# Optimization experiments

Hardware: AMD Instinct MI355X
Metric: run time of the kernel (lower is better)

The kernel has to match this reference:

```python
import jax, jax.numpy as jnp
import numpy as np

N_HEAD = 16

def setup_inputs() -> dict:
    key = jax.random.key(0)
    ks = jax.random.split(key, 5)
    d = 1024
    x = jax.random.normal(ks[0], (2, 2048, d), dtype=jnp.float32)
    Wqkv = jax.random.normal(ks[1], (d, 3 * d), dtype=jnp.float32) * (1.0 / np.sqrt(d))
    bqkv = jnp.zeros((3 * d,), dtype=jnp.float32)
    Wproj = jax.random.normal(ks[2], (d, d), dtype=jnp.float32) * (1.0 / np.sqrt(d))
    bproj = jnp.zeros((d,), dtype=jnp.float32)
    return {"x": x, "Wqkv": Wqkv, "bqkv": bqkv, "Wproj": Wproj, "bproj": bproj}


def reference(x, Wqkv, bqkv, Wproj, bproj):
    B, T, C = x.shape
    H = N_HEAD
    Dh = C // H
    qkv = x @ Wqkv + bqkv                      # [B, T, 3C]
    q, k, v = jnp.split(qkv, 3, axis=-1)
    # [B, T, C] -> [B, H, T, Dh]
    q = q.reshape(B, T, H, Dh).transpose(0, 2, 1, 3)
    k = k.reshape(B, T, H, Dh).transpose(0, 2, 1, 3)
    v = v.reshape(B, T, H, Dh).transpose(0, 2, 1, 3)
    scale = 1.0 / np.sqrt(Dh)
    att = jnp.einsum('bhqd,bhkd->bhqk', q, k) * scale
    causal = jnp.tril(jnp.ones((T, T), dtype=bool))
    att = jnp.where(causal[None, None, :, :], att, jnp.float32(-jnp.inf))
    att = jax.nn.softmax(att, axis=-1)
    y = jnp.einsum('bhqk,bhkd->bhqd', att, v)  # [B, H, T, Dh]
    y = y.transpose(0, 2, 1, 3).reshape(B, T, C)
    return y @ Wproj + bproj
```

## Files before the change

### kernel.cpp

```cpp
#include <hip/hip_runtime.h>
#include <math.h>


typedef __attribute__((ext_vector_type(8))) short short8;
typedef __attribute__((ext_vector_type(4))) short short4v;
typedef __attribute__((ext_vector_type(4))) float floatx4;

__device__ __forceinline__ unsigned short f2bf(float f) {
  unsigned u = __float_as_uint(f);
  return (unsigned short)((u + 0x7fff + ((u >> 16) & 1)) >> 16);
}

__device__ __forceinline__ void pack_a_body(const float* __restrict__ in,
                                            unsigned short* __restrict__ out,
                                            int K, int m0, int k0,
                                            unsigned short (*lds)[72], int t) {
  {
    int ml = t >> 2, kl = (t & 3) * 16;
    const float4* p = (const float4*)(in + (size_t)(m0 + ml) * K + k0 + kl);
    unsigned short* q = &lds[ml][kl];
#pragma unroll
    for (int c = 0; c < 4; ++c) {
      float4 v = p[c];
      q[c * 4 + 0] = f2bf(v.x);
      q[c * 4 + 1] = f2bf(v.y);
      q[c * 4 + 2] = f2bf(v.z);
      q[c * 4 + 3] = f2bf(v.w);
    }
  }
  __syncthreads();
  int chunk = t >> 3, sub = t & 7;
  int mt = chunk >> 3, kc = chunk & 7;
  unsigned short tmp[16];
#pragma unroll
  for (int j2 = 0; j2 < 2; ++j2)
#pragma unroll
    for (int j = 0; j < 8; ++j)
      tmp[j2 * 8 + j] = lds[mt * 16 + sub * 2 + j2][kc * 8 + j];
  size_t ofs = ((size_t)(m0 >> 4) + mt) * (16 * (size_t)K) +
               ((size_t)(k0 >> 3) + kc) * 128 + sub * 16;
  *(int4*)(out + ofs) = *(int4*)(tmp);
  *(int4*)(out + ofs + 8) = *(int4*)(tmp + 8);
}

__device__ __forceinline__ void pack_bt_body(const float* __restrict__ in,
                                             unsigned short* __restrict__ out,
                                             int K, int N, int n0, int k0,
                                             unsigned short (*lds)[72], int t) {
  {
    int kl = t >> 2, nl = (t & 3) * 16;
    const float4* p = (const float4*)(in + (size_t)(k0 + kl) * N + n0 + nl);
#pragma unroll
    for (int c = 0; c < 4; ++c) {
      float4 v = p[c];
      lds[nl + c * 4 + 0][kl] = f2bf(v.x);
      lds[nl + c * 4 + 1][kl] = f2bf(v.y);
      lds[nl + c * 4 + 2][kl] = f2bf(v.z);
      lds[nl + c * 4 + 3][kl] = f2bf(v.w);
    }
  }
  __syncthreads();
  int chunk = t >> 3, sub = t & 7;
  int nt = chunk >> 3, kc = chunk & 7;
  unsigned short tmp[16];
#pragma unroll
  for (int j2 = 0; j2 < 2; ++j2)
#pragma unroll
    for (int j = 0; j < 8; ++j)
      tmp[j2 * 8 + j] = lds[nt * 16 + sub * 2 + j2][kc * 8 + j];
  size_t ofs = ((size_t)(n0 >> 4) + nt) * (16 * (size_t)K) +
               ((size_t)(k0 >> 3) + kc) * 128 + sub * 16;
  *(int4*)(out + ofs) = *(int4*)(tmp);
  *(int4*)(out + ofs + 8) = *(int4*)(tmp + 8);
}

__global__ __launch_bounds__(256) void pack_all(
    const float* __restrict__ x, const float* __restrict__ Wqkv,
    const float* __restrict__ Wproj, unsigned short* __restrict__ xbf,
    unsigned short* __restrict__ wqkvF, unsigned short* __restrict__ wprojF) {
  __shared__ __align__(16) unsigned short lds[64][72];
  const int b = blockIdx.x, t = threadIdx.x;
  if (b < 1024) {
    pack_a_body(x, xbf, 1024, (b >> 4) * 64, (b & 15) * 64, lds, t);
  } else if (b < 1792) {
    int b2 = b - 1024;
    pack_bt_body(Wqkv, wqkvF, 1024, 3072, (b2 % 48) * 64, (b2 / 48) * 64, lds, t);
  } else {
    int b3 = b - 1792;
    pack_bt_body(Wproj, wprojF, 1024, 1024, (b3 & 15) * 64, (b3 >> 4) * 64, lds, t);
  }
}

template <int MODE, int IM>
__global__ __launch_bounds__(256) void gemm_frag(
    const unsigned short* __restrict__ A, const unsigned short* __restrict__ B,
    const float* __restrict__ bias, float* __restrict__ Cout,
    unsigned short* __restrict__ Qb, unsigned short* __restrict__ Kb,
    unsigned short* __restrict__ Vt, int M, int N, int K) {
  const int tid = threadIdx.x;
  const int wave = tid >> 6, lane = tid & 63;
  const int quad = lane >> 4, l15 = lane & 15;
  const int nbands = M / (IM * 16);
  const int band = (int)(blockIdx.x % nbands);
  const int grp = (int)(blockIdx.x / nbands);
  const int m0 = band * (IM * 16);
  const int n0 = (grp * 4 + wave) * 64;
  const int lofs = quad * 128 + l15 * 8;

  const unsigned short* pA[IM];
  const unsigned short* pB[4];
#pragma unroll
  for (int im = 0; im < IM; ++im)
    pA[im] = A + ((size_t)(m0 >> 4) + im) * (16 * (size_t)K) + lofs;
#pragma unroll
  for (int in = 0; in < 4; ++in)
    pB[in] = B + ((size_t)(n0 >> 4) + in) * (16 * (size_t)K) + lofs;

  floatx4 acc[IM][4];
#pragma unroll
  for (int i = 0; i < IM; ++i)
#pragma unroll
    for (int j = 0; j < 4; ++j) acc[i][j] = (floatx4)0.0f;

  const int nk = K >> 6;
  short8 fa[IM][2], fb[4][2], ga[IM][2], gb[4][2];

#pragma unroll
  for (int im = 0; im < IM; ++im) {
    fa[im][0] = *(const short8*)(pA[im]);
    fa[im][1] = *(const short8*)(pA[im] + 512);
  }
#pragma unroll
  for (int in = 0; in < 4; ++in) {
    fb[in][0] = *(const short8*)(pB[in]);
    fb[in][1] = *(const short8*)(pB[in] + 512);
  }

  for (int ki = 0; ki < nk; ki += 2) {
#pragma unroll
    for (int im = 0; im < IM; ++im) {
      ga[im][0] = *(const short8*)(pA[im] + 1024);
      ga[im][1] = *(const short8*)(pA[im] + 1536);
    }
#pragma unroll
    for (int in = 0; in < 4; ++in) {
      gb[in][0] = *(const short8*)(pB[in] + 1024);
      gb[in][1] = *(const short8*)(pB[in] + 1536);
    }
#pragma unroll
    for (int ks = 0; ks < 2; ++ks)
#pragma unroll
      for (int im = 0; im < IM; ++im)
#pragma unroll
        for (int in = 0; in < 4; ++in)
          acc[im][in] = __builtin_amdgcn_mfma_f32_16x16x32_bf16(
              fa[im][ks], fb[in][ks], acc[im][in], 0, 0, 0);
#pragma unroll
    for (int im = 0; im < IM; ++im) pA[im] += 2048;
#pragma unroll
    for (int in = 0; in < 4; ++in) pB[in] += 2048;
    if (ki + 2 < nk) {
#pragma unroll
      for (int im = 0; im < IM; ++im) {
        fa[im][0] = *(const short8*)(pA[im]);
        fa[im][1] = *(const short8*)(pA[im] + 512);
      }
#pragma unroll
      for (int in = 0; in < 4; ++in) {
        fb[in][0] = *(const short8*)(pB[in]);
        fb[in][1] = *(const short8*)(pB[in] + 512);
      }
    }
#pragma unroll
    for (int ks = 0; ks < 2; ++ks)
#pragma unroll
      for (int im = 0; im < IM; ++im)
#pragma unroll
        for (int in = 0; in < 4; ++in)
          acc[im][in] = __builtin_amdgcn_mfma_f32_16x16x32_bf16(
              ga[im][ks], gb[in][ks], acc[im][in], 0, 0, 0);
  }

  if (MODE == 0) {
    const float QSCALE = 0.18033688f;
#pragma unroll
    for (int im = 0; im < IM; ++im) {
      int mbase = m0 + im * 16 + quad * 4;
      int bb = mbase >> 11, tb = mbase & 2047;
#pragma unroll
      for (int in = 0; in < 4; ++in) {
        int n = n0 + in * 16 + l15;
        float bv = bias[n];
        int which = n >> 10;
        int h = (n >> 6) & 15;
        int d = n & 63;
        size_t bh_ = (size_t)(bb * 16 + h);
        if (which == 2) {
          size_t base = bh_ * 131072 + (size_t)(d >> 4) * 32768 +
                        (size_t)(tb >> 3) * 128 + (d & 15) * 8 + (tb & 7);
          short4v pk;
#pragma unroll
          for (int r = 0; r < 4; ++r) pk[r] = (short)f2bf(acc[im][in][r] + bv);
          *(short4v*)(Vt + base) = pk;
        } else {
          size_t base = bh_ * 131072 + (size_t)(tb >> 4) * 1024 +
                        (d >> 3) * 128 + (tb & 15) * 8 + (d & 7);
          if (which == 0) {
#pragma unroll
            for (int r = 0; r < 4; ++r)
              Qb[base + r * 8] = f2bf((acc[im][in][r] + bv) * QSCALE);
          } else {
#pragma unroll
            for (int r = 0; r < 4; ++r)
              Kb[base + r * 8] = f2bf(acc[im][in][r] + bv);
          }
        }
      }
    }
  } else {
#pragma unroll
    for (int im = 0; im < IM; ++im) {
      int mbase = m0 + im * 16 + quad * 4;
#pragma unroll
      for (int in = 0; in < 4; ++in) {
        int n = n0 + in * 16 + l15;
        float bv = bias[n];
#pragma unroll
        for (int r = 0; r < 4; ++r)
          Cout[(size_t)(mbase + r) * N + n] = acc[im][in][r] + bv;
      }
    }
  }
}

__global__ __launch_bounds__(256) void attn_mfma(
    const unsigned short* __restrict__ Q, const unsigned short* __restrict__ K,
    const unsigned short* __restrict__ Vt, unsigned short* __restrict__ Y) {
  const int bh = blockIdx.x;
  const int wave = threadIdx.x >> 6;
  const int lane = threadIdx.x & 63;
  const int s = ((int)(gridDim.y - 1 - blockIdx.y)) * 4 + wave;
  const int quad = lane >> 4, l15 = lane & 15;

  __shared__ __align__(16) unsigned short Plds[4][16][72];
  unsigned short(*P)[72] = Plds[wave];

  const int t0 = s * 16;
  const unsigned short* Qb = Q + (size_t)bh * 131072;
  const unsigned short* Kb = K + (size_t)bh * 131072;
  const unsigned short* Vb = Vt + (size_t)bh * 131072;
  const int lofs = quad * 128 + l15 * 8;

  short8 qf[2];
#pragma unroll
  for (int c = 0; c < 2; ++c)
    qf[c] = *(const short8*)(Qb + (size_t)s * 1024 + c * 512 + lofs);

  floatx4 o[4];
#pragma unroll
  for (int in = 0; in < 4; ++in) o[in] = (floatx4)0.0f;
  float l_acc = 0.f;

  const int ntiles = (s >> 2) + 1;

  short8 kf[4][2], vf[4][2];
#pragma unroll
  for (int in = 0; in < 4; ++in) {
    const unsigned short* kp = Kb + (size_t)in * 1024 + lofs;
    kf[in][0] = *(const short8*)(kp);
    kf[in][1] = *(const short8*)(kp + 512);
  }

  for (int jt = 0; jt < ntiles; ++jt) {
    const int kt0 = jt * 64;
#pragma unroll
    for (int in = 0; in < 4; ++in) {
      const unsigned short* vp =
          Vb + (size_t)in * 32768 + (size_t)jt * 1024 + lofs;
      vf[in][0] = *(const short8*)(vp);
      vf[in][1] = *(const short8*)(vp + 512);
    }

    floatx4 sa[4];
#pragma unroll
    for (int in = 0; in < 4; ++in) {
      floatx4 z = (floatx4)0.0f;
      z = __builtin_amdgcn_mfma_f32_16x16x32_bf16(kf[in][0], qf[0], z, 0, 0, 0);
      sa[in] = __builtin_amdgcn_mfma_f32_16x16x32_bf16(kf[in][1], qf[1], z, 0, 0, 0);
    }

    if (jt + 1 < ntiles) {
#pragma unroll
      for (int in = 0; in < 4; ++in) {
        const unsigned short* kp = Kb + (size_t)(jt * 4 + 4 + in) * 1024 + lofs;
        kf[in][0] = *(const short8*)(kp);
        kf[in][1] = *(const short8*)(kp + 512);
      }
    }

    if (jt == ntiles - 1) {
#pragma unroll
      for (int in = 0; in < 4; ++in) {
        int keyb = kt0 + in * 16 + quad * 4;
#pragma unroll
        for (int r = 0; r < 4; ++r)
          if (keyb + r > t0 + l15) sa[in][r] = -__builtin_inff();
      }
    }

#pragma unroll
    for (int in = 0; in < 4; ++in)
#pragma unroll
      for (int r = 0; r < 4; ++r) {
        float p = exp2f(sa[in][r]);
        sa[in][r] = p;
        l_acc += p;
      }

#pragma unroll
    for (int in = 0; in < 4; ++in) {
      uint2 pk;
      pk.x = (__float_as_uint(sa[in][0]) >> 16) |
             (__float_as_uint(sa[in][1]) & 0xFFFF0000u);
      pk.y = (__float_as_uint(sa[in][2]) >> 16) |
             (__float_as_uint(sa[in][3]) & 0xFFFF0000u);
      *(uint2*)&P[l15][in * 16 + quad * 4] = pk;
    }
    short8 pf0 = *(const short8*)&P[l15][quad * 8];
    short8 pf1 = *(const short8*)&P[l15][32 + quad * 8];

#pragma unroll
    for (int in = 0; in < 4; ++in) {
      o[in] = __builtin_amdgcn_mfma_f32_16x16x32_bf16(pf0, vf[in][0], o[in], 0, 0, 0);
      o[in] = __builtin_amdgcn_mfma_f32_16x16x32_bf16(pf1, vf[in][1], o[in], 0, 0, 0);
    }
  }

  l_acc += __shfl_xor(l_acc, 16);
  l_acc += __shfl_xor(l_acc, 32);

  const int b_ = bh >> 4, h = bh & 15;
  float inv[4];
#pragma unroll
  for (int r = 0; r < 4; ++r)
    inv[r] = 1.f / __shfl(l_acc, (lane & 48) | (quad * 4 + r));

  size_t mt = (size_t)(b_ * 128 + s);
#pragma unroll
  for (int in = 0; in < 4; ++in) {
    size_t cbase = (size_t)(h * 8 + in * 2 + (l15 >> 3)) * 128 + (l15 & 7);
#pragma unroll
    for (int r = 0; r < 4; ++r)
      Y[mt * 16384 + cbase + (quad * 4 + r) * 8] = f2bf(o[in][r] * inv[r]);
  }
}

extern "C" void kernel_launch(void* const* d_in, const int* in_sizes, int n_in,
                              void* d_out, int out_size, void* d_ws,
                              size_t ws_size, hipStream_t stream) {
  const float* x = (const float*)d_in[0];
  const float* Wqkv = (const float*)d_in[1];
  const float* bqkv = (const float*)d_in[2];
  const float* Wproj = (const float*)d_in[3];
  const float* bproj = (const float*)d_in[4];
  float* out = (float*)d_out;

  const int C = 1024;
  const int M = 4096;

  char* ws = (char*)d_ws;
  unsigned short* qbuf = (unsigned short*)ws;
  unsigned short* kbuf = (unsigned short*)(ws + 8388608);
  unsigned short* vtbuf = (unsigned short*)(ws + 16777216);
  unsigned short* ybuf = (unsigned short*)(ws + 25165824);
  unsigned short* xbf = (unsigned short*)(ws + 33554432);
  unsigned short* wqkvF = (unsigned short*)(ws + 41943040);
  unsigned short* wprojF = (unsigned short*)(ws + 48234496);

  dim3 blk(256);
  pack_all<<<dim3(2048), blk, 0, stream>>>(x, Wqkv, Wproj, xbf, wqkvF, wprojF);
  gemm_frag<0, 4><<<dim3((M / 64) * (3 * C / 256)), blk, 0, stream>>>(
      xbf, wqkvF, bqkv, nullptr, qbuf, kbuf, vtbuf, M, 3 * C, C);
  attn_mfma<<<dim3(32, 32), blk, 0, stream>>>(qbuf, kbuf, vtbuf, ybuf);
  gemm_frag<1, 2><<<dim3((M / 32) * (C / 256)), blk, 0, stream>>>(
      ybuf, wprojF, bproj, out, nullptr, nullptr, nullptr, M, C, C);
}
```

Before: 189.3 us.

## Stage GEMM tiles through LDS with direct global-to-LDS loads and XCD-aware mapping

Replaces the register-only fragment GEMM, where each wave loaded its own A and B fragments from global memory, with a 128x128 block tile staged in shared memory. The tiles are filled by global_load_lds and then shared by the four waves in a 2x2 arrangement. Block indices are remapped so that column groups stay on the same XCD, which should improve L2 reuse. The aim is to cut redundant global traffic. In exchange there is a barrier every K-step and no double buffering, so load latency is no longer overlapped with MFMA work.

```diff
diff --git a/kernel.cpp b/kernel.cpp
--- a/kernel.cpp
+++ b/kernel.cpp
@@ -9,6 +9,12 @@
 __device__ __forceinline__ unsigned short f2bf(float f) {
   unsigned u = __float_as_uint(f);
   return (unsigned short)((u + 0x7fff + ((u >> 16) & 1)) >> 16);
+}
+
+__device__ __forceinline__ void gld16(const unsigned short* g, unsigned short* l) {
+  __builtin_amdgcn_global_load_lds(
+      (const __attribute__((address_space(1))) unsigned int*)g,
+      (__attribute__((address_space(3))) unsigned int*)l, 16, 0, 0);
 }
 
 __device__ __forceinline__ void pack_a_body(const float* __restrict__ in,
@@ -91,8 +97,8 @@
   }
 }
 
-template <int MODE, int IM>
-__global__ __launch_bounds__(256) void gemm_frag(
+template <int MODE>
+__global__ __launch_bounds__(256, 3) void gemm_lds(
     const unsigned short* __restrict__ A, const unsigned short* __restrict__ B,
     const float* __restrict__ bias, float* __restrict__ Cout,
     unsigned short* __restrict__ Qb, unsigned short* __restrict__ Kb,
@@ -100,96 +106,82 @@
   const int tid = threadIdx.x;
   const int wave = tid >> 6, lane = tid & 63;
   const int quad = lane >> 4, l15 = lane & 15;
-  const int nbands = M / (IM * 16);
-  const int band = (int)(blockIdx.x % nbands);
-  const int grp = (int)(blockIdx.x / nbands);
-  const int m0 = band * (IM * 16);
-  const int n0 = (grp * 4 + wave) * 64;
-  const int lofs = quad * 128 + l15 * 8;
-
-  const unsigned short* pA[IM];
-  const unsigned short* pB[4];
-#pragma unroll
-  for (int im = 0; im < IM; ++im)
-    pA[im] = A + ((size_t)(m0 >> 4) + im) * (16 * (size_t)K) + lofs;
-#pragma unroll
-  for (int in = 0; in < 4; ++in)
-    pB[in] = B + ((size_t)(n0 >> 4) + in) * (16 * (size_t)K) + lofs;
-
-  floatx4 acc[IM][4];
-#pragma unroll
-  for (int i = 0; i < IM; ++i)
+  const int wr = wave >> 1, wc = wave & 1;
+
+  const int nbn = N >> 7;
+  const int colsPerX = nbn >> 3;
+  const int xcd = (int)(blockIdx.x & 7);
+  const int idx = (int)(blockIdx.x >> 3);
+  const int bn = xcd * colsPerX + (colsPerX == 1 ? 0 : (idx % colsPerX));
+  const int bm = (colsPerX == 1) ? idx : (idx / colsPerX);
+
+  const int mt0 = bm * 8;
+  const int nt0 = bn * 8;
+
+  __shared__ __align__(16) unsigned short As[8192];
+  __shared__ __align__(16) unsigned short Bs[8192];
+
+  const unsigned short* spA[4];
+  const unsigned short* spB[4];
+#pragma unroll
+  for (int j = 0; j < 4; ++j) {
+    int c = wave * 4 + j;
+    spA[j] = A + ((size_t)(mt0 + (c >> 1))) * (16 * (size_t)K) +
+             (c & 1) * 512 + lane * 8;
+    spB[j] = B + ((size_t)(nt0 + (c >> 1))) * (16 * (size_t)K) +
+             (c & 1) * 512 + lane * 8;
+  }
+
+  floatx4 acc[4][4];
+#pragma unroll
+  for (int i = 0; i < 4; ++i)
 #pragma unroll
     for (int j = 0; j < 4; ++j) acc[i][j] = (floatx4)0.0f;
 
+  const int fofs = quad * 128 + l15 * 8;
   const int nk = K >> 6;
-  short8 fa[IM][2], fb[4][2], ga[IM][2], gb[4][2];
-
-#pragma unroll
-  for (int im = 0; im < IM; ++im) {
-    fa[im][0] = *(const short8*)(pA[im]);
-    fa[im][1] = *(const short8*)(pA[im] + 512);
-  }
-#pragma unroll
-  for (int in = 0; in < 4; ++in) {
-    fb[in][0] = *(const short8*)(pB[in]);
-    fb[in][1] = *(const short8*)(pB[in] + 512);
-  }
-
-  for (int ki = 0; ki < nk; ki += 2) {
-#pragma unroll
-    for (int im = 0; im < IM; ++im) {
-      ga[im][0] = *(const short8*)(pA[im] + 1024);
-      ga[im][1] = *(const short8*)(pA[im] + 1536);
-    }
-#pragma unroll
-    for (int in = 0; in < 4; ++in) {
-      gb[in][0] = *(const short8*)(pB[in] + 1024);
-      gb[in][1] = *(const short8*)(pB[in] + 1536);
-    }
-#pragma unroll
-    for (int ks = 0; ks < 2; ++ks)
-#pragma unroll
-      for (int im = 0; im < IM; ++im)
+
+  for (int kk = 0; kk < nk; ++kk) {
+#pragma unroll
+    for (int j = 0; j < 4; ++j) {
+      gld16(spA[j], &As[(wave * 4 + j) * 512]);
+      gld16(spB[j], &Bs[(wave * 4 + j) * 512]);
+      spA[j] += 1024;
+      spB[j] += 1024;
+    }
+    __syncthreads();
+
+#pragma unroll
+    for (int ks = 0; ks < 2; ++ks) {
+      short8 fa[4], fb[4];
+#pragma unroll
+      for (int im = 0; im < 4; ++im)
+        fa[im] = *(const short8*)&As[((wr * 4 + im) * 2 + ks) * 512 + fofs];
+#pragma unroll
+      for (int in = 0; in < 4; ++in)
+        fb[in] = *(const short8*)&Bs[((wc * 4 + in) * 2 + ks) * 512 + fofs];
+#pragma unroll
+      for (int im = 0; im < 4; ++im)
 #pragma unroll
         for (int in = 0; in < 4; ++in)
           acc[im][in] = __builtin_amdgcn_mfma_f32_16x16x32_bf16(
-              fa[im][ks], fb[in][ks], acc[im][in], 0, 0, 0);
-#pragma unroll
-    for (int im = 0; im < IM; ++im) pA[im] += 2048;
-#pragma unroll
-    for (int in = 0; in < 4; ++in) pB[in] += 2048;
-    if (ki + 2 < nk) {
-#pragma unroll
-      for (int im = 0; im < IM; ++im) {
-        fa[im][0] = *(const short8*)(pA[im]);
-        fa[im][1] = *(const short8*)(pA[im] + 512);
-      }
-#pragma unroll
-      for (int in = 0; in < 4; ++in) {
-        fb[in][0] = *(const short8*)(pB[in]);
-        fb[in][1] = *(const short8*)(pB[in] + 512);
-      }
-    }
-#pragma unroll
-    for (int ks = 0; ks < 2; ++ks)
-#pragma unroll
-      for (int im = 0; im < IM; ++im)
-#pragma unroll
-        for (int in = 0; in < 4; ++in)
-          acc[im][in] = __builtin_amdgcn_mfma_f32_16x16x32_bf16(
-              ga[im][ks], gb[in][ks], acc[im][in], 0, 0, 0);
-  }
+              fa[im], fb[in], acc[im][in], 0, 0, 0);
+    }
+    if (kk + 1 < nk) __syncthreads();
+  }
+
+  const int m0w = bm * 128 + wr * 64;
+  const int n0w = bn * 128 + wc * 64;
 
   if (MODE == 0) {
     const float QSCALE = 0.18033688f;
 #pragma unroll
-    for (int im = 0; im < IM; ++im) {
-      int mbase = m0 + im * 16 + quad * 4;
+    for (int im = 0; im < 4; ++im) {
+      int mbase = m0w + im * 16 + quad * 4;
       int bb = mbase >> 11, tb = mbase & 2047;
 #pragma unroll
       for (int in = 0; in < 4; ++in) {
-        int n = n0 + in * 16 + l15;
+        int n = n0w + in * 16 + l15;
         float bv = bias[n];
         int which = n >> 10;
         int h = (n >> 6) & 15;
@@ -219,11 +211,11 @@
     }
   } else {
 #pragma unroll
-    for (int im = 0; im < IM; ++im) {
-      int mbase = m0 + im * 16 + quad * 4;
+    for (int im = 0; im < 4; ++im) {
+      int mbase = m0w + im * 16 + quad * 4;
 #pragma unroll
       for (int in = 0; in < 4; ++in) {
-        int n = n0 + in * 16 + l15;
+        int n = n0w + in * 16 + l15;
         float bv = bias[n];
 #pragma unroll
         for (int r = 0; r < 4; ++r)
@@ -379,9 +371,9 @@
 
   dim3 blk(256);
   pack_all<<<dim3(2048), blk, 0, stream>>>(x, Wqkv, Wproj, xbf, wqkvF, wprojF);
-  gemm_frag<0, 4><<<dim3((M / 64) * (3 * C / 256)), blk, 0, stream>>>(
+  gemm_lds<0><<<dim3((M / 128) * (3 * C / 128)), blk, 0, stream>>>(
       xbf, wqkvF, bqkv, nullptr, qbuf, kbuf, vtbuf, M, 3 * C, C);
   attn_mfma<<<dim3(32, 32), blk, 0, stream>>>(qbuf, kbuf, vtbuf, ybuf);
-  gemm_frag<1, 2><<<dim3((M / 32) * (C / 256)), blk, 0, stream>>>(
+  gemm_lds<1><<<dim3((M / 128) * (C / 128)), blk, 0, stream>>>(
       ybuf, wprojF, bproj, out, nullptr, nullptr, nullptr, M, C, C);
 }
```

Result: faster. 180.9 us (-4.5%).
